# Kernel optimization log

Measured on AMD Instinct MI355X. Metric: run time of the kernel, lower is better.

The kernel has to match this reference:

```python
import jax, jax.numpy as jnp
import numpy as np
from jax import lax


def _sobel():
    kx = jnp.array([[1., 0., -1.], [2., 0., -2.], [1., 0., -1.]], dtype=jnp.float32) / 4.0
    ky = jnp.array([[1., 2., 1.], [0., 0., 0.], [-1., -2., -1.]], dtype=jnp.float32) / 4.0
    return kx, ky


def _depthwise(x, k2d):
    # x: [B,C,H,W]; k2d: [3,3] -> grouped conv with one filter per channel
    C = x.shape[1]
    k = jnp.tile(k2d[None, None].astype(x.dtype), (C, 1, 1, 1))  # [C,1,3,3]
    return lax.conv_general_dilated(x, k, (1, 1), ((1, 1), (1, 1)),
                                    feature_group_count=C,
                                    dimension_numbers=('NCHW', 'OIHW', 'NCHW'))


def setup_inputs() -> dict:
    key = jax.random.key(0)
    ks = jax.random.split(key, 5)
    B, C, H, W = 8, 256, 160, 160
    hidden = max(8, C // 16)  # 16
    ksize = 7
    x = jax.random.normal(ks[0], (B, C, H, W), dtype=jnp.float32)
    w1 = jax.random.normal(ks[1], (hidden, C), dtype=jnp.float32) * (1.0 / np.sqrt(C))
    w2 = jax.random.normal(ks[2], (C, hidden), dtype=jnp.float32) * (1.0 / np.sqrt(hidden))
    spatial_w = jax.random.normal(ks[3], (1, 4, ksize, ksize), dtype=jnp.float32) * (1.0 / np.sqrt(4 * ksize * ksize))
    spatial_b = jnp.zeros((1,), dtype=jnp.float32)
    alpha = jnp.zeros((), dtype=jnp.float32)
    beta = jnp.zeros((), dtype=jnp.float32)
    return {"x": x, "w1": w1, "w2": w2, "spatial_w": spatial_w,
            "spatial_b": spatial_b, "alpha": alpha, "beta": beta}


def reference(x, w1, w2, spatial_w, spatial_b, alpha, beta):
    kx, ky = _sobel()
    gx = _depthwise(x, kx)
    gy = _depthwise(x, ky)
    g = jnp.sqrt(gx * gx + gy * gy + 1e-12)            # [B,C,H,W]

    # channel gate: mean edge magnitude per channel -> small MLP -> sigmoid
    c_vec = g.mean(axis=(-1, -2))                       # [B,C]
    h = jax.nn.relu(c_vec @ w1.T)                       # [B,hidden]
    w = jax.nn.sigmoid(h @ w2.T)[:, :, None, None]      # [B,C,1,1]

    # spatial gate: 4-channel descriptor -> 7x7 conv -> sigmoid
    avg_x = x.mean(axis=1, keepdims=True)
    max_x = x.max(axis=1, keepdims=True)
    avg_g = g.mean(axis=1, keepdims=True)
    max_g = g.max(axis=1, keepdims=True)
    s_in = jnp.concatenate([avg_x, max_x, avg_g, max_g], axis=1)  # [B,4,H,W]
    pad = spatial_w.shape[-1] // 2
    s = lax.conv_general_dilated(s_in, spatial_w, (1, 1), ((pad, pad), (pad, pad)),
                                 dimension_numbers=('NCHW', 'OIHW', 'NCHW'))
    s = jax.nn.sigmoid(s + spatial_b[None, :, None, None])        # [B,1,H,W]

    a = jax.nn.softplus(alpha)
    b = jax.nn.softplus(beta)
    return x * (1.0 + a * s) * (1.0 + b * w)
```

## Files before the change

kernel.cpp:

```cpp
#include <hip/hip_runtime.h>
#include <math.h>

#define B 8
#define C 256
#define H 160
#define W 160
#define HW (H*W)
#define HIDDEN 16

#define CCHUNK 32
#define NCHUNK (C/CCHUNK)
#define GRP 4
#define BLKT 128
#define W4 (W/4)
#define F4B (HW/4)
#define PBB (F4B/BLKT)
#define PBLKS (B*PBB)
#define FOLDBLKS ((B*4*F4B)/256)

__device__ __forceinline__ float sobel4_core(
    float tl, float4 t4, float tr,
    float ml, float4 m4, float mr,
    float bl, float4 b4, float br,
    float4& sum_x, float4& max_x, float4& sum_g, float4& max_g)
{
    const float rt_[6] = { tl, t4.x, t4.y, t4.z, t4.w, tr };
    const float rm_[6] = { ml, m4.x, m4.y, m4.z, m4.w, mr };
    const float rb_[6] = { bl, b4.x, b4.y, b4.z, b4.w, br };
    float g4[4];
    #pragma unroll
    for (int i = 0; i < 4; ++i) {
        float u = (rt_[i]-rt_[i+2]) + 2.f*(rm_[i]-rm_[i+2]) + (rb_[i]-rb_[i+2]);
        float v = (rt_[i]+2.f*rt_[i+1]+rt_[i+2]) - (rb_[i]+2.f*rb_[i+1]+rb_[i+2]);
        g4[i] = 0.25f * __builtin_amdgcn_sqrtf(fmaf(v, v, fmaf(u, u, 1.6e-11f)));
    }
    sum_x.x += m4.x; sum_x.y += m4.y; sum_x.z += m4.z; sum_x.w += m4.w;
    max_x.x = fmaxf(max_x.x, m4.x); max_x.y = fmaxf(max_x.y, m4.y);
    max_x.z = fmaxf(max_x.z, m4.z); max_x.w = fmaxf(max_x.w, m4.w);
    sum_g.x += g4[0]; sum_g.y += g4[1]; sum_g.z += g4[2]; sum_g.w += g4[3];
    max_g.x = fmaxf(max_g.x, g4[0]); max_g.y = fmaxf(max_g.y, g4[1]);
    max_g.z = fmaxf(max_g.z, g4[2]); max_g.w = fmaxf(max_g.w, g4[3]);
    return (g4[0]+g4[1]) + (g4[2]+g4[3]);
}

__global__ __launch_bounds__(BLKT, 5) void k1_sobel_stats(
    const float* __restrict__ x, float* __restrict__ part_c,
    float* __restrict__ part_s)
{
    const int tid   = threadIdx.x;
    const int blk   = blockIdx.x;
    const int chunk = blk & (NCHUNK-1);
    const int pblk  = blk >> 3;
    const int f     = pblk * BLKT + tid;
    const int b     = f / F4B;
    const int r     = f % F4B;
    const int h     = r / W4;
    const int w     = (r % W4) * 4;
    const int hw    = h * W + w;

    const bool up = (h > 0), dn = (h < H-1), lf = (w > 0), rt = (w+4 < W);
    const float lff = lf ? 1.f : 0.f, rtf = rt ? 1.f : 0.f;

    const float* xp = x + (size_t)(b*C + chunk*CCHUNK) * HW + hw;
    float* pcw = part_c + ((size_t)blk*2 + (tid >> 6)) * CCHUNK;

    float4 sum_x = {0,0,0,0}, sum_g = {0,0,0,0};
    float4 max_x = {-INFINITY,-INFINITY,-INFINITY,-INFINITY};
    float4 max_g = {-INFINITY,-INFINITY,-INFINITY,-INFINITY};

    if (__all(up && dn)) {
        #pragma unroll 1
        for (int grp = 0; grp < CCHUNK/GRP; ++grp) {
            float gs[GRP];
            #pragma unroll
            for (int u = 0; u < GRP; ++u) {
                const float* q = xp + (size_t)(grp*GRP + u) * HW;
                float4 t4 = *(const float4*)(q - W);
                float4 m4 = *(const float4*)(q);
                float4 b4 = *(const float4*)(q + W);
                float tl = q[-W-1]*lff, tr = q[-W+4]*rtf;
                float ml = q[-1]  *lff, mr = q[4]   *rtf;
                float bl = q[W-1] *lff, br = q[W+4] *rtf;
                gs[u] = sobel4_core(tl,t4,tr, ml,m4,mr, bl,b4,br,
                                    sum_x, max_x, sum_g, max_g);
            }
            #pragma unroll
            for (int off = 32; off; off >>= 1) {
                #pragma unroll
                for (int u = 0; u < GRP; ++u)
                    gs[u] += __shfl_xor(gs[u], off, 64);
            }
            if ((tid & 63) == 0) {
                float4 v0 = { gs[0], gs[1], gs[2], gs[3] };
                *(float4*)(pcw + grp*GRP) = v0;
            }
        }
    } else {
        const float upf = up ? 1.f : 0.f, dnf = dn ? 1.f : 0.f;
        const float f_tl = upf*lff, f_tr = upf*rtf;
        const float f_bl = dnf*lff, f_br = dnf*rtf;
        const int ot = up ? -W : 0;
        const int ob = dn ?  W : 0;
        const int ol = lf ? -1 : 0;
        const int orr= rt ?  4 : 3;

        #pragma unroll 1
        for (int grp = 0; grp < CCHUNK/GRP; ++grp) {
            float gs[GRP];
            #pragma unroll
            for (int u = 0; u < GRP; ++u) {
                const float* q = xp + (size_t)(grp*GRP + u) * HW;
                float4 t4 = *(const float4*)(q + ot);
                float4 m4 = *(const float4*)(q);
                float4 b4 = *(const float4*)(q + ob);
                float tl = q[ot+ol]*f_tl, tr = q[ot+orr]*f_tr;
                float ml = q[ol]  *lff,   mr = q[orr]  *rtf;
                float bl = q[ob+ol]*f_bl, br = q[ob+orr]*f_br;
                t4.x*=upf; t4.y*=upf; t4.z*=upf; t4.w*=upf;
                b4.x*=dnf; b4.y*=dnf; b4.z*=dnf; b4.w*=dnf;
                gs[u] = sobel4_core(tl,t4,tr, ml,m4,mr, bl,b4,br,
                                    sum_x, max_x, sum_g, max_g);
            }
            #pragma unroll
            for (int off = 32; off; off >>= 1) {
                #pragma unroll
                for (int u = 0; u < GRP; ++u)
                    gs[u] += __shfl_xor(gs[u], off, 64);
            }
            if ((tid & 63) == 0) {
                float4 v0 = { gs[0], gs[1], gs[2], gs[3] };
                *(float4*)(pcw + grp*GRP) = v0;
            }
        }
    }

    float* sp = part_s + (size_t)(chunk*B + b) * 4 * HW + hw;
    *(float4*)(sp)        = sum_x;
    *(float4*)(sp +   HW) = max_x;
    *(float4*)(sp + 2*HW) = sum_g;
    *(float4*)(sp + 3*HW) = max_g;
}

__global__ __launch_bounds__(256) void k1b_fold_mlp(
    const float* __restrict__ part_s, float* __restrict__ s_in,
    const float* __restrict__ part_c, const float* __restrict__ w1,
    const float* __restrict__ w2, const float* __restrict__ beta,
    float* __restrict__ chanfac)
{
    __shared__ float cv[C];
    __shared__ float hb[HIDDEN];
    const int tid = threadIdx.x;

    if (blockIdx.x < FOLDBLKS) {
        const int g    = blockIdx.x * 256 + tid;
        const int b    = g / (4*F4B);
        const int rr   = g % (4*F4B);
        const int plane= rr / F4B;
        const int hw   = (rr % F4B) * 4;

        const float* sp0 = part_s + (size_t)b * 4 * HW + plane*HW + hw;
        const size_t cstride = (size_t)B * 4 * HW;

        float4 v = *(const float4*)(sp0);
        if (plane == 0 || plane == 2) {
            #pragma unroll
            for (int c = 1; c < NCHUNK; ++c) {
                float4 u = *(const float4*)(sp0 + c*cstride);
                v.x += u.x; v.y += u.y; v.z += u.z; v.w += u.w;
            }
            v.x *= (1.f/C); v.y *= (1.f/C); v.z *= (1.f/C); v.w *= (1.f/C);
        } else {
            #pragma unroll
            for (int c = 1; c < NCHUNK; ++c) {
                float4 u = *(const float4*)(sp0 + c*cstride);
                v.x = fmaxf(v.x,u.x); v.y = fmaxf(v.y,u.y);
                v.z = fmaxf(v.z,u.z); v.w = fmaxf(v.w,u.w);
            }
        }
        *(float4*)(s_in + (size_t)b * 4 * HW + plane*HW + hw) = v;
        return;
    }

    const int b     = blockIdx.x - FOLDBLKS;
    const int chunk = tid >> 5;
    const int cc    = tid & (CCHUNK-1);

    float acc = 0.f;
    for (int pbb = 0; pbb < PBB; ++pbb) {
        const int blk = (b*PBB + pbb) * NCHUNK + chunk;
        const float* pcb = part_c + (size_t)blk * 2 * CCHUNK + cc;
        acc += pcb[0] + pcb[CCHUNK];
    }
    cv[tid] = acc * (1.f/(float)HW);
    __syncthreads();

    if (tid < HIDDEN) {
        float a = 0.f;
        for (int c = 0; c < C; ++c) a += cv[c] * w1[tid*C + c];
        hb[tid] = fmaxf(a, 0.f);
    }
    __syncthreads();

    float bt = beta[0];
    float sb = (bt > 20.f) ? bt : log1pf(expf(bt));
    float a = 0.f;
    #pragma unroll
    for (int j = 0; j < HIDDEN; ++j) a += hb[j] * w2[tid*HIDDEN + j];
    float gate = 1.f / (1.f + expf(-a));
    chanfac[b*C + tid] = 1.f + sb * gate;
}

__global__ __launch_bounds__(256) void k3_spatial(
    const float* __restrict__ s_in, const float* __restrict__ sw,
    const float* __restrict__ sbias, const float* __restrict__ alpha,
    float* __restrict__ sfac)
{
    __shared__ float wgt[4*49];
    const int tid = threadIdx.x;
    if (tid < 196) wgt[tid] = sw[tid];
    __syncthreads();

    const int p  = blockIdx.x * 256 + tid;
    const int b  = p / HW;
    const int hw = p % HW;
    const int h  = hw / W;
    const int w  = hw % W;

    int wc[7]; float wm[7];
    #pragma unroll
    for (int j = 0; j < 7; ++j) {
        int ww = w + j - 3;
        wm[j] = (ww >= 0 && ww < W) ? 1.f : 0.f;
        wc[j] = min(max(ww, 0), W-1) - w;
    }
    int hc[7]; float hm[7];
    #pragma unroll
    for (int i = 0; i < 7; ++i) {
        int hh = h + i - 3;
        hm[i] = (hh >= 0 && hh < H) ? 1.f : 0.f;
        hc[i] = min(max(hh, 0), H-1);
    }

    const float* base = s_in + (size_t)b * 4 * HW + w;
    float acc = 0.f;
    #pragma unroll
    for (int ci = 0; ci < 4; ++ci) {
        const float* pl = base + ci*HW;
        #pragma unroll
        for (int i = 0; i < 7; ++i) {
            const float* row = pl + hc[i]*W;
            const float* wr  = wgt + ci*49 + i*7;
            float racc = 0.f;
            #pragma unroll
            for (int j = 0; j < 7; ++j)
                racc = fmaf(wr[j], row[wc[j]] * wm[j], racc);
            acc = fmaf(racc, hm[i], acc);
        }
    }
    float al = alpha[0];
    float sa = (al > 20.f) ? al : log1pf(expf(al));
    float sg = 1.f / (1.f + expf(-(acc + sbias[0])));
    sfac[p] = 1.f + sa * sg;
}

__global__ __launch_bounds__(256) void k4_combine(
    const float4* __restrict__ x4, const float* __restrict__ sfac,
    const float* __restrict__ chanfac, float4* __restrict__ out4)
{
    const int i0 = blockIdx.x * 512 + threadIdx.x;
    #pragma unroll
    for (int k = 0; k < 2; ++k) {
        const int i  = i0 + k*256;
        const int e  = i * 4;
        const int bc = e / HW;
        const int hw = e % HW;
        const int b  = bc / C;

        const float cf = chanfac[bc];
        const float4 s = *(const float4*)&sfac[b*HW + hw];
        float4 xv = x4[i];
        float4 o;
        o.x = xv.x * s.x * cf;
        o.y = xv.y * s.y * cf;
        o.z = xv.z * s.z * cf;
        o.w = xv.w * s.w * cf;
        out4[i] = o;
    }
}

extern "C" void kernel_launch(void* const* d_in, const int* in_sizes, int n_in,
                              void* d_out, int out_size, void* d_ws, size_t ws_size,
                              hipStream_t stream) {
    const float* x     = (const float*)d_in[0];
    const float* w1    = (const float*)d_in[1];
    const float* w2    = (const float*)d_in[2];
    const float* sw    = (const float*)d_in[3];
    const float* sbias = (const float*)d_in[4];
    const float* alpha = (const float*)d_in[5];
    const float* beta  = (const float*)d_in[6];
    float* out = (float*)d_out;

    float* ws = (float*)d_ws;
    float* part_c  = ws;
    float* part_s  = part_c + (size_t)PBLKS*NCHUNK*2*CCHUNK;
    float* s_in    = part_s + (size_t)NCHUNK*B*4*HW;
    float* sfac    = s_in   + (size_t)B*4*HW;
    float* chanfac = sfac   + (size_t)B*HW;

    k1_sobel_stats<<<PBLKS*NCHUNK, BLKT, 0, stream>>>(x, part_c, part_s);
    k1b_fold_mlp <<<FOLDBLKS + B,  256, 0, stream>>>(part_s, s_in, part_c, w1, w2, beta, chanfac);
    k3_spatial   <<<(B*HW)/256,    256, 0, stream>>>(s_in, sw, sbias, alpha, sfac);
    k4_combine   <<<(B*C*HW/4)/512, 256, 0, stream>>>((const float4*)x, sfac, chanfac, (float4*)out);
}
```

Measured before the change: 565.6 us.

## Separate Sobel arithmetic, enlarge stats blocks, vectorize 7x7 spatial conv to four outputs

The Sobel core now computes the vertical smoothing and difference sums once per column and reuses them across the four outputs, which cuts ALU work. The stats kernel moves from 128 to 256 threads per block and drops the occupancy hint, so the channel partials grow to four wave slots per block and the fold kernel sums four entries instead of two. The spatial 7x7 conv now has each thread produce four adjacent outputs from float4 row loads, reusing loaded columns in registers, and writes them with one float4 store. Risks are register pressure and occupancy changes in the larger stats kernel, plus far fewer threads in the spatial kernel.

```diff
diff --git a/kernel.cpp b/kernel.cpp
--- a/kernel.cpp
+++ b/kernel.cpp
@@ -11,39 +11,51 @@
 #define CCHUNK 32
 #define NCHUNK (C/CCHUNK)
 #define GRP 4
-#define BLKT 128
 #define W4 (W/4)
 #define F4B (HW/4)
-#define PBB (F4B/BLKT)
+#define PBB (F4B/256)
 #define PBLKS (B*PBB)
 #define FOLDBLKS ((B*4*F4B)/256)
 
-__device__ __forceinline__ float sobel4_core(
+__device__ __forceinline__ float sobel4_sep(
     float tl, float4 t4, float tr,
     float ml, float4 m4, float mr,
     float bl, float4 b4, float br,
     float4& sum_x, float4& max_x, float4& sum_g, float4& max_g)
 {
-    const float rt_[6] = { tl, t4.x, t4.y, t4.z, t4.w, tr };
-    const float rm_[6] = { ml, m4.x, m4.y, m4.z, m4.w, mr };
-    const float rb_[6] = { bl, b4.x, b4.y, b4.z, b4.w, br };
-    float g4[4];
-    #pragma unroll
-    for (int i = 0; i < 4; ++i) {
-        float u = (rt_[i]-rt_[i+2]) + 2.f*(rm_[i]-rm_[i+2]) + (rb_[i]-rb_[i+2]);
-        float v = (rt_[i]+2.f*rt_[i+1]+rt_[i+2]) - (rb_[i]+2.f*rb_[i+1]+rb_[i+2]);
-        g4[i] = 0.25f * __builtin_amdgcn_sqrtf(fmaf(v, v, fmaf(u, u, 1.6e-11f)));
-    }
+    float s0 = fmaf(2.f, ml,   tl)   + bl;
+    float s1 = fmaf(2.f, m4.x, t4.x) + b4.x;
+    float s2 = fmaf(2.f, m4.y, t4.y) + b4.y;
+    float s3 = fmaf(2.f, m4.z, t4.z) + b4.z;
+    float s4 = fmaf(2.f, m4.w, t4.w) + b4.w;
+    float s5 = fmaf(2.f, mr,   tr)   + br;
+    float d0 = tl   - bl;
+    float d1 = t4.x - b4.x;
+    float d2 = t4.y - b4.y;
+    float d3 = t4.z - b4.z;
+    float d4 = t4.w - b4.w;
+    float d5 = tr   - br;
+
+    float g0, g1, g2, g3;
+    { float u = s0 - s2, v = fmaf(2.f, d1, d0) + d2;
+      g0 = 0.25f * __builtin_amdgcn_sqrtf(fmaf(v, v, fmaf(u, u, 1.6e-11f))); }
+    { float u = s1 - s3, v = fmaf(2.f, d2, d1) + d3;
+      g1 = 0.25f * __builtin_amdgcn_sqrtf(fmaf(v, v, fmaf(u, u, 1.6e-11f))); }
+    { float u = s2 - s4, v = fmaf(2.f, d3, d2) + d4;
+      g2 = 0.25f * __builtin_amdgcn_sqrtf(fmaf(v, v, fmaf(u, u, 1.6e-11f))); }
+    { float u = s3 - s5, v = fmaf(2.f, d4, d3) + d5;
+      g3 = 0.25f * __builtin_amdgcn_sqrtf(fmaf(v, v, fmaf(u, u, 1.6e-11f))); }
+
     sum_x.x += m4.x; sum_x.y += m4.y; sum_x.z += m4.z; sum_x.w += m4.w;
     max_x.x = fmaxf(max_x.x, m4.x); max_x.y = fmaxf(max_x.y, m4.y);
     max_x.z = fmaxf(max_x.z, m4.z); max_x.w = fmaxf(max_x.w, m4.w);
-    sum_g.x += g4[0]; sum_g.y += g4[1]; sum_g.z += g4[2]; sum_g.w += g4[3];
-    max_g.x = fmaxf(max_g.x, g4[0]); max_g.y = fmaxf(max_g.y, g4[1]);
-    max_g.z = fmaxf(max_g.z, g4[2]); max_g.w = fmaxf(max_g.w, g4[3]);
-    return (g4[0]+g4[1]) + (g4[2]+g4[3]);
-}
-
-__global__ __launch_bounds__(BLKT, 5) void k1_sobel_stats(
+    sum_g.x += g0; sum_g.y += g1; sum_g.z += g2; sum_g.w += g3;
+    max_g.x = fmaxf(max_g.x, g0); max_g.y = fmaxf(max_g.y, g1);
+    max_g.z = fmaxf(max_g.z, g2); max_g.w = fmaxf(max_g.w, g3);
+    return (g0+g1) + (g2+g3);
+}
+
+__global__ __launch_bounds__(256) void k1_sobel_stats(
     const float* __restrict__ x, float* __restrict__ part_c,
     float* __restrict__ part_s)
 {
@@ -51,7 +63,7 @@
     const int blk   = blockIdx.x;
     const int chunk = blk & (NCHUNK-1);
     const int pblk  = blk >> 3;
-    const int f     = pblk * BLKT + tid;
+    const int f     = pblk * 256 + tid;
     const int b     = f / F4B;
     const int r     = f % F4B;
     const int h     = r / W4;
@@ -62,7 +74,7 @@
     const float lff = lf ? 1.f : 0.f, rtf = rt ? 1.f : 0.f;
 
     const float* xp = x + (size_t)(b*C + chunk*CCHUNK) * HW + hw;
-    float* pcw = part_c + ((size_t)blk*2 + (tid >> 6)) * CCHUNK;
+    float* pcw = part_c + ((size_t)blk*4 + (tid >> 6)) * CCHUNK;
 
     float4 sum_x = {0,0,0,0}, sum_g = {0,0,0,0};
     float4 max_x = {-INFINITY,-INFINITY,-INFINITY,-INFINITY};
@@ -81,8 +93,8 @@
                 float tl = q[-W-1]*lff, tr = q[-W+4]*rtf;
                 float ml = q[-1]  *lff, mr = q[4]   *rtf;
                 float bl = q[W-1] *lff, br = q[W+4] *rtf;
-                gs[u] = sobel4_core(tl,t4,tr, ml,m4,mr, bl,b4,br,
-                                    sum_x, max_x, sum_g, max_g);
+                gs[u] = sobel4_sep(tl,t4,tr, ml,m4,mr, bl,b4,br,
+                                   sum_x, max_x, sum_g, max_g);
             }
             #pragma unroll
             for (int off = 32; off; off >>= 1) {
@@ -118,8 +130,8 @@
                 float bl = q[ob+ol]*f_bl, br = q[ob+orr]*f_br;
                 t4.x*=upf; t4.y*=upf; t4.z*=upf; t4.w*=upf;
                 b4.x*=dnf; b4.y*=dnf; b4.z*=dnf; b4.w*=dnf;
-                gs[u] = sobel4_core(tl,t4,tr, ml,m4,mr, bl,b4,br,
-                                    sum_x, max_x, sum_g, max_g);
+                gs[u] = sobel4_sep(tl,t4,tr, ml,m4,mr, bl,b4,br,
+                                   sum_x, max_x, sum_g, max_g);
             }
             #pragma unroll
             for (int off = 32; off; off >>= 1) {
@@ -188,8 +200,8 @@
     float acc = 0.f;
     for (int pbb = 0; pbb < PBB; ++pbb) {
         const int blk = (b*PBB + pbb) * NCHUNK + chunk;
-        const float* pcb = part_c + (size_t)blk * 2 * CCHUNK + cc;
-        acc += pcb[0] + pcb[CCHUNK];
+        const float* pcb = part_c + (size_t)blk * 4 * CCHUNK + cc;
+        acc += (pcb[0] + pcb[CCHUNK]) + (pcb[2*CCHUNK] + pcb[3*CCHUNK]);
     }
     cv[tid] = acc * (1.f/(float)HW);
     __syncthreads();
@@ -210,28 +222,27 @@
     chanfac[b*C + tid] = 1.f + sb * gate;
 }
 
-__global__ __launch_bounds__(256) void k3_spatial(
+__global__ __launch_bounds__(64) void k3_spatial(
     const float* __restrict__ s_in, const float* __restrict__ sw,
     const float* __restrict__ sbias, const float* __restrict__ alpha,
     float* __restrict__ sfac)
 {
     __shared__ float wgt[4*49];
     const int tid = threadIdx.x;
-    if (tid < 196) wgt[tid] = sw[tid];
+    for (int k = tid; k < 196; k += 64) wgt[k] = sw[k];
     __syncthreads();
 
-    const int p  = blockIdx.x * 256 + tid;
-    const int b  = p / HW;
-    const int hw = p % HW;
-    const int h  = hw / W;
-    const int w  = hw % W;
-
-    int wc[7]; float wm[7];
-    #pragma unroll
-    for (int j = 0; j < 7; ++j) {
-        int ww = w + j - 3;
-        wm[j] = (ww >= 0 && ww < W) ? 1.f : 0.f;
-        wc[j] = min(max(ww, 0), W-1) - w;
+    const int p4 = blockIdx.x * 64 + tid;
+    const int b  = p4 / F4B;
+    const int r  = p4 % F4B;
+    const int h  = r / W4;
+    const int w  = (r % W4) * 4;
+
+    float wmk[11];
+    #pragma unroll
+    for (int k = 1; k <= 10; ++k) {
+        int col = w - 4 + k;
+        wmk[k] = (col >= 0 && col < W) ? 1.f : 0.f;
     }
     int hc[7]; float hm[7];
     #pragma unroll
@@ -240,27 +251,48 @@
         hm[i] = (hh >= 0 && hh < H) ? 1.f : 0.f;
         hc[i] = min(max(hh, 0), H-1);
     }
+    const int loff = (w >= 4)    ? -4 : 0;
+    const int roff = (w + 4 < W) ?  4 : 0;
 
     const float* base = s_in + (size_t)b * 4 * HW + w;
-    float acc = 0.f;
+    float a0=0.f, a1=0.f, a2=0.f, a3=0.f;
     #pragma unroll
     for (int ci = 0; ci < 4; ++ci) {
         const float* pl = base + ci*HW;
         #pragma unroll
         for (int i = 0; i < 7; ++i) {
-            const float* row = pl + hc[i]*W;
-            const float* wr  = wgt + ci*49 + i*7;
-            float racc = 0.f;
-            #pragma unroll
-            for (int j = 0; j < 7; ++j)
-                racc = fmaf(wr[j], row[wc[j]] * wm[j], racc);
-            acc = fmaf(racc, hm[i], acc);
+            const float* rp = pl + hc[i]*W;
+            float4 L  = *(const float4*)(rp + loff);
+            float4 Mv = *(const float4*)(rp);
+            float4 R  = *(const float4*)(rp + roff);
+            float rb[12] = { L.x,L.y,L.z,L.w, Mv.x,Mv.y,Mv.z,Mv.w, R.x,R.y,R.z,R.w };
+            #pragma unroll
+            for (int k = 1; k <= 10; ++k) rb[k] *= wmk[k];
+            const float* wr = wgt + ci*49 + i*7;
+            float r0=0.f, r1=0.f, r2=0.f, r3=0.f;
+            #pragma unroll
+            for (int j = 0; j < 7; ++j) {
+                float wj = wr[j];
+                r0 = fmaf(wj, rb[j+1], r0);
+                r1 = fmaf(wj, rb[j+2], r1);
+                r2 = fmaf(wj, rb[j+3], r2);
+                r3 = fmaf(wj, rb[j+4], r3);
+            }
+            a0 = fmaf(r0, hm[i], a0);
+            a1 = fmaf(r1, hm[i], a1);
+            a2 = fmaf(r2, hm[i], a2);
+            a3 = fmaf(r3, hm[i], a3);
         }
     }
     float al = alpha[0];
     float sa = (al > 20.f) ? al : log1pf(expf(al));
-    float sg = 1.f / (1.f + expf(-(acc + sbias[0])));
-    sfac[p] = 1.f + sa * sg;
+    float bias = sbias[0];
+    float4 o;
+    o.x = 1.f + sa / (1.f + expf(-(a0 + bias)));
+    o.y = 1.f + sa / (1.f + expf(-(a1 + bias)));
+    o.z = 1.f + sa / (1.f + expf(-(a2 + bias)));
+    o.w = 1.f + sa / (1.f + expf(-(a3 + bias)));
+    *(float4*)(sfac + (size_t)b * HW + h*W + w) = o;
 }
 
 __global__ __launch_bounds__(256) void k4_combine(
@@ -302,13 +334,13 @@
 
     float* ws = (float*)d_ws;
     float* part_c  = ws;
-    float* part_s  = part_c + (size_t)PBLKS*NCHUNK*2*CCHUNK;
+    float* part_s  = part_c + (size_t)PBLKS*NCHUNK*4*CCHUNK;
     float* s_in    = part_s + (size_t)NCHUNK*B*4*HW;
     float* sfac    = s_in   + (size_t)B*4*HW;
     float* chanfac = sfac   + (size_t)B*HW;
 
-    k1_sobel_stats<<<PBLKS*NCHUNK, BLKT, 0, stream>>>(x, part_c, part_s);
+    k1_sobel_stats<<<PBLKS*NCHUNK, 256, 0, stream>>>(x, part_c, part_s);
     k1b_fold_mlp <<<FOLDBLKS + B,  256, 0, stream>>>(part_s, s_in, part_c, w1, w2, beta, chanfac);
-    k3_spatial   <<<(B*HW)/256,    256, 0, stream>>>(s_in, sw, sbias, alpha, sfac);
+    k3_spatial   <<<(B*F4B)/64,    64,  0, stream>>>(s_in, sw, sbias, alpha, sfac);
     k4_combine   <<<(B*C*HW/4)/512, 256, 0, stream>>>((const float4*)x, sfac, chanfac, (float4*)out);
 }
```

Result: faster. 464.6 us (-17.9%).
